# Kernel tuning notes

Measured on AMD Instinct MI355X. Metric: run time of the kernel, lower is better.

## Reference

```python
import jax, jax.numpy as jnp
import numpy as np

N, M, N0 = 100000, 12, 2500            # atoms, max neighbors, crystals
ORIG, C, NBR, H, NCONV = 92, 64, 41, 128, 3
EPS = 1e-5                              # torch BatchNorm1d default eps


def setup_inputs() -> dict:
    key = jax.random.key(0)
    ks = jax.random.split(key, 10)
    return {
        "atom_fea": jax.random.normal(ks[0], (N, ORIG), jnp.float32),
        "nbr_fea": jax.random.normal(ks[1], (N, M, NBR), jnp.float32),
        "nbr_fea_idx": jax.random.randint(ks[2], (N, M), 0, N),
        "crystal_atom_idx": jnp.sort(jax.random.randint(ks[3], (N,), 0, N0)),
        # learned parameters (Linear weights stored as (in, out))
        "emb_W": jax.random.normal(ks[4], (ORIG, C), jnp.float32) * 0.05,
        "emb_b": jnp.zeros((C,), jnp.float32),
        "fc_W": jax.random.normal(ks[5], (NCONV, 2 * C + NBR, 2 * C), jnp.float32) * 0.05,
        "fc_b": jnp.zeros((NCONV, 2 * C), jnp.float32),
        "bn1_g": jnp.ones((NCONV, 2 * C), jnp.float32),
        "bn1_b": jnp.zeros((NCONV, 2 * C), jnp.float32),
        "bn2_g": jnp.ones((NCONV, C), jnp.float32),
        "bn2_b": jnp.zeros((NCONV, C), jnp.float32),
        "head_W": jax.random.normal(ks[6], (C, H), jnp.float32) * 0.05,
        "head_b": jnp.zeros((H,), jnp.float32),
        "out_W": jax.random.normal(ks[7], (H, 1), jnp.float32) * 0.05,
        "out_b": jnp.zeros((1,), jnp.float32),
    }


def _bn(x, g, b):
    # training-mode BatchNorm1d: per-feature batch mean/var (biased)
    mu = jnp.mean(x, axis=0)
    var = jnp.var(x, axis=0)
    return (x - mu) * jax.lax.rsqrt(var + EPS) * g + b


def reference(atom_fea, nbr_fea, nbr_fea_idx, crystal_atom_idx,
              emb_W, emb_b, fc_W, fc_b, bn1_g, bn1_b, bn2_g, bn2_b,
              head_W, head_b, out_W, out_b):
    h = atom_fea @ emb_W + emb_b                       # (N, C)
    for l in range(NCONV):
        nbr_h = h[nbr_fea_idx]                         # gather (N, M, C)
        self_h = jnp.broadcast_to(h[:, None, :], (N, M, C))
        tot = jnp.concatenate([self_h, nbr_h, nbr_fea], axis=2)  # (N, M, 2C+NBR)
        g = tot @ fc_W[l] + fc_b[l]                    # (N, M, 2C)
        g = _bn(g.reshape(-1, 2 * C), bn1_g[l], bn1_b[l]).reshape(N, M, 2 * C)
        filt = jax.nn.sigmoid(g[..., :C])
        core = jax.nn.softplus(g[..., C:])
        summed = jnp.sum(filt * core, axis=1)          # (N, C)
        summed = _bn(summed, bn2_g[l], bn2_b[l])
        h = jax.nn.softplus(h + summed)                # residual
    # per-crystal mean pooling via segment sum
    counts = jax.ops.segment_sum(jnp.ones((N,), h.dtype), crystal_atom_idx, num_segments=N0)
    crys = jax.ops.segment_sum(h, crystal_atom_idx, num_segments=N0) / jnp.maximum(counts, 1.0)[:, None]
    z = jax.nn.softplus(jax.nn.softplus(crys) @ head_W + head_b)  # (N0, H)
    return z @ out_W + out_b                            # (N0, 1)
```

## Files before the change

### kernel.cpp

```cpp
#include <hip/hip_runtime.h>

#define NA 100000
#define MN 12
#define KE 41
#define N0C 2500
#define EPSBN 1e-5f
#define ROWDW 24
#define CONV_BLOCKS 1536
#define CONV_WAVES (CONV_BLOCKS * 4)

typedef _Float16 h2v __attribute__((ext_vector_type(2)));
typedef _Float16 h8v __attribute__((ext_vector_type(8)));
typedef float f4v __attribute__((ext_vector_type(4)));
typedef unsigned int uint;
union H2U { uint u; h2v h; };

__device__ __forceinline__ float softplusf(float x){
  float e = __expf(-fabsf(x));
  return fmaxf(x, 0.f) + __logf(1.f + e);
}
__device__ __forceinline__ float sigmoidf(float x){
  return __fdividef(1.f, 1.f + __expf(-x));
}
__device__ __forceinline__ int waveid(){
  return __builtin_amdgcn_readfirstlane((int)((blockIdx.x * blockDim.x + threadIdx.x) >> 6));
}

__global__ __launch_bounds__(256) void k_cast_e(const float* __restrict__ e,
                                                uint* __restrict__ EF)
{
  const int TOT = NA * MN * ROWDW;
  for (int i = blockIdx.x * 256 + threadIdx.x; i < TOT; i += gridDim.x * 256) {
    int r = i / ROWDW, k2 = i - r * ROWDW;
    const float* row = e + (size_t)r * KE;
    float a = 0.f, b = 0.f;
    if (k2 < 20) { a = row[2 * k2]; b = row[2 * k2 + 1]; }
    else if (k2 == 20) { a = row[40]; }
    H2U cv; cv.h = h2v{(_Float16)a, (_Float16)b};
    EF[i] = cv.u;
  }
}

__global__ __launch_bounds__(256) void k_embed(const float* __restrict__ af,
                                               const float* __restrict__ W,
                                               const float* __restrict__ b,
                                               float* __restrict__ h, int nw)
{
  int t = threadIdx.x & 63;
  int wid = waveid();
  float bias = b[t];
  for (int n0 = wid * 2; n0 < NA; n0 += nw * 2) {
    int n1 = n0 + 1;
    bool has1 = (n1 < NA);
    const float* a0 = af + (size_t)n0 * 92;
    const float* a1 = af + (size_t)(has1 ? n1 : n0) * 92;
    float acc0 = bias, acc1 = bias;
#pragma unroll 4
    for (int k = 0; k < 92; ++k) {
      float w = W[k * 64 + t];
      acc0 += a0[k] * w;
      acc1 += a1[k] * w;
    }
    h[(size_t)n0 * 64 + t] = acc0;
    if (has1) h[(size_t)n1 * 64 + t] = acc1;
  }
}

template<int FUSE>
__global__ __launch_bounds__(256) void k_hw(float* __restrict__ h,
                                            const float* __restrict__ summed,
                                            const float* __restrict__ scsh2,
                                            const float* __restrict__ fcW,
                                            uint* __restrict__ hWs,
                                            uint* __restrict__ hWn, int nw)
{
  __shared__ float Wl[64 * 256];
  for (int i = threadIdx.x; i < 64 * 256; i += 256) {
    int c = i >> 8, q = i & 255;
    int j = q & 63, part = q >> 6;
    Wl[(c * 64 + j) * 4 + part] = fcW[(c + ((part >> 1) << 6)) * 128 + ((part & 1) << 6) + j];
  }
  __syncthreads();
  int t = threadIdx.x & 63;
  int wid = waveid();
  float sc = 0.f, sh = 0.f;
  if (FUSE) { sc = scsh2[t]; sh = scsh2[64 + t]; }
  const float4* W4 = (const float4*)Wl;
  for (int n0 = wid * 2; n0 < NA; n0 += nw * 2) {
    int n1 = n0 + 1;
    bool has1 = (n1 < NA);
    float hf0 = h[(size_t)n0 * 64 + t];
    float hf1 = h[(size_t)(has1 ? n1 : n0) * 64 + t];
    if (FUSE) {
      hf0 = softplusf(hf0 + summed[(size_t)n0 * 64 + t] * sc + sh);
      hf1 = softplusf(hf1 + summed[(size_t)(has1 ? n1 : n0) * 64 + t] * sc + sh);
      h[(size_t)n0 * 64 + t] = hf0;
      if (has1) h[(size_t)n1 * 64 + t] = hf1;
    }
    float4 A = {0,0,0,0}, B = {0,0,0,0};
#pragma unroll 4
    for (int c = 0; c < 64; ++c) {
      float4 w = W4[c * 64 + t];
      float x0 = __shfl(hf0, c, 64);
      float x1 = __shfl(hf1, c, 64);
      A.x += x0 * w.x; A.y += x0 * w.y; A.z += x0 * w.z; A.w += x0 * w.w;
      B.x += x1 * w.x; B.y += x1 * w.y; B.z += x1 * w.z; B.w += x1 * w.w;
    }
    H2U p0, p1;
    p0.h = h2v{(_Float16)A.x, (_Float16)A.y};
    p1.h = h2v{(_Float16)A.z, (_Float16)A.w};
    hWs[(size_t)n0 * 64 + t] = p0.u;
    hWn[(size_t)n0 * 64 + t] = p1.u;
    if (has1) {
      p0.h = h2v{(_Float16)B.x, (_Float16)B.y};
      p1.h = h2v{(_Float16)B.z, (_Float16)B.w};
      hWs[(size_t)n1 * 64 + t] = p0.u;
      hWn[(size_t)n1 * 64 + t] = p1.u;
    }
  }
}

template<int APPLY>
__global__ __launch_bounds__(256) void k_conv(const uint* __restrict__ EF,
                                              const uint* __restrict__ hWs,
                                              const uint* __restrict__ hWn,
                                              const int*  __restrict__ idx,
                                              const float* __restrict__ We,
                                              const float* __restrict__ scsh,
                                              float* __restrict__ summed,
                                              float* __restrict__ stats)
{
  __shared__ float gt_all[4][12 * 132];
  int l = threadIdx.x & 63;
  int w = threadIdx.x >> 6;
  float* gt = gt_all[w];
  int wid = __builtin_amdgcn_readfirstlane(blockIdx.x * 4 + w);
  int c16 = l & 15, kg = l >> 4;

  h8v b1[8], b2[8];
#pragma unroll
  for (int T = 0; T < 8; ++T) {
    h8v v1 = {0,0,0,0,0,0,0,0}, v2 = {0,0,0,0,0,0,0,0};
#pragma unroll
    for (int j = 0; j < 8; ++j)
      v1[j] = (_Float16)We[(kg * 8 + j) * 128 + T * 16 + c16];
    if (kg < 2) {
#pragma unroll
      for (int j = 0; j < 8; ++j) {
        int k = 32 + kg * 8 + j;
        v2[j] = (k < KE) ? (_Float16)We[k * 128 + T * 16 + c16] : (_Float16)0.f;
      }
    }
    b1[T] = v1; b2[T] = v2;
  }

  float sc0 = 0, sh0 = 0, sc1 = 0, sh1 = 0;
  if (APPLY) { sc0 = scsh[l]; sc1 = scsh[l + 64]; sh0 = scsh[128 + l]; sh1 = scsh[192 + l]; }
  float s0 = 0, q0 = 0, s1 = 0, q1 = 0;

  for (int n = wid; n < NA; n += CONV_WAVES) {
    const uint* ep = EF + (size_t)n * (MN * ROWDW);
    h8v a1 = {0,0,0,0,0,0,0,0}, a2 = {0,0,0,0,0,0,0,0};
    if (c16 < MN) {
      a1 = *(const h8v*)(ep + c16 * ROWDW + kg * 4);
      if (kg < 2) a2 = *(const h8v*)(ep + c16 * ROWDW + 16 + kg * 4);
    }
    const int* ip = idx + n * MN;
    H2U sp; sp.u = hWs[(size_t)n * 64 + l];
    uint nbp[MN];
#pragma unroll
    for (int m = 0; m < MN; ++m) nbp[m] = hWn[(size_t)ip[m] * 64 + l];

    f4v acc[8];
#pragma unroll
    for (int T = 0; T < 8; ++T) acc[T] = f4v{0.f, 0.f, 0.f, 0.f};
#pragma unroll
    for (int T = 0; T < 8; ++T)
      acc[T] = __builtin_amdgcn_mfma_f32_16x16x32_f16(a1, b1[T], acc[T], 0, 0, 0);
#pragma unroll
    for (int T = 0; T < 8; ++T)
      acc[T] = __builtin_amdgcn_mfma_f32_16x16x32_f16(a2, b2[T], acc[T], 0, 0, 0);

    if (kg < 3) {
#pragma unroll
      for (int T = 0; T < 8; ++T)
#pragma unroll
        for (int r = 0; r < 4; ++r)
          gt[(kg * 4 + r) * 132 + T * 16 + c16] = acc[T][r];
    }

    float self0 = (float)sp.h[0], self1 = (float)sp.h[1];
    float accsum = 0.f;
#pragma unroll
    for (int m = 0; m < MN; ++m) {
      H2U nv; nv.u = nbp[m];
      float g0 = gt[m * 132 + l]      + self0 + (float)nv.h[0];
      float g1 = gt[m * 132 + 64 + l] + self1 + (float)nv.h[1];
      if (APPLY) {
        float f  = sigmoidf(g0 * sc0 + sh0);
        float cr = softplusf(g1 * sc1 + sh1);
        accsum += f * cr;
      } else {
        s0 += g0; q0 += g0 * g0;
        s1 += g1; q1 += g1 * g1;
      }
    }
    if (APPLY) {
      summed[(size_t)n * 64 + l] = accsum;
      s0 += accsum; q0 += accsum * accsum;
    }
  }
  if (APPLY) {
    atomicAdd(&stats[l], s0);
    atomicAdd(&stats[64 + l], q0);
  } else {
    atomicAdd(&stats[l], s0);
    atomicAdd(&stats[64 + l], s1);
    atomicAdd(&stats[128 + l], q0);
    atomicAdd(&stats[192 + l], q1);
  }
}

__global__ void k_fin1(const float* __restrict__ st, const float* __restrict__ g,
                       const float* __restrict__ b, float* __restrict__ scsh)
{
  int j = threadIdx.x;
  float inv = 1.f / (float)(NA * MN);
  float mean = st[j] * inv;
  float var  = st[128 + j] * inv - mean * mean;
  float rstd = rsqrtf(var + EPSBN);
  float sc = g[j] * rstd;
  scsh[j] = sc;
  scsh[128 + j] = b[j] - mean * sc;
}
__global__ void k_fin2(const float* __restrict__ st, const float* __restrict__ g,
                       const float* __restrict__ b, float* __restrict__ scsh)
{
  int j = threadIdx.x;
  float inv = 1.f / (float)NA;
  float mean = st[j] * inv;
  float var  = st[64 + j] * inv - mean * mean;
  float rstd = rsqrtf(var + EPSBN);
  float sc = g[j] * rstd;
  scsh[j] = sc;
  scsh[64 + j] = b[j] - mean * sc;
}

__global__ __launch_bounds__(256) void k_bn2res(float* __restrict__ h,
                                                const float* __restrict__ summed,
                                                const float* __restrict__ scsh)
{
  int tot = NA * 64 / 4;
  const float4* s4 = (const float4*)summed;
  float4* h4 = (float4*)h;
  for (int i = blockIdx.x * blockDim.x + threadIdx.x; i < tot; i += gridDim.x * blockDim.x) {
    int c4 = i & 15;
    float4 sc = ((const float4*)scsh)[c4];
    float4 sh = ((const float4*)(scsh + 64))[c4];
    float4 hv = h4[i], sv = s4[i];
    hv.x = softplusf(hv.x + sv.x * sc.x + sh.x);
    hv.y = softplusf(hv.y + sv.y * sc.y + sh.y);
    hv.z = softplusf(hv.z + sv.z * sc.z + sh.z);
    hv.w = softplusf(hv.w + sv.w * sc.w + sh.w);
    h4[i] = hv;
  }
}

__global__ __launch_bounds__(256) void k_pool(const float* __restrict__ h,
                                              const int* __restrict__ cidx,
                                              float* __restrict__ csum,
                                              float* __restrict__ ccnt, int nw)
{
  int t = threadIdx.x & 63;
  int wid = waveid();
  int chunk = (NA + nw - 1) / nw;
  int n0 = wid * chunk;
  int n1 = min(n0 + chunk, NA);
  if (n0 >= NA) return;
  float acc = 0.f, cacc = 0.f;
  int cur = -1;
  for (int n = n0; n < n1; ++n) {
    int ci = cidx[n];
    if (ci != cur) {
      if (cur >= 0) {
        atomicAdd(&csum[(size_t)cur * 64 + t], acc);
        if (t == 0) atomicAdd(&ccnt[cur], cacc);
      }
      cur = ci; acc = 0.f; cacc = 0.f;
    }
    acc += h[(size_t)n * 64 + t];
    cacc += 1.f;
  }
  if (cur >= 0) {
    atomicAdd(&csum[(size_t)cur * 64 + t], acc);
    if (t == 0) atomicAdd(&ccnt[cur], cacc);
  }
}

__global__ __launch_bounds__(256) void k_head(const float* __restrict__ csum,
                                              const float* __restrict__ ccnt,
                                              const float* __restrict__ Wh,
                                              const float* __restrict__ bh,
                                              const float* __restrict__ Wo,
                                              const float* __restrict__ bo,
                                              float* __restrict__ out)
{
  __shared__ float Wl[64 * 128];
  for (int i = threadIdx.x; i < 64 * 128; i += 256) Wl[i] = Wh[i];
  __syncthreads();
  int t = threadIdx.x & 63;
  int ci = blockIdx.x * 4 + (threadIdx.x >> 6);
  if (ci >= N0C) return;
  float cnt = fmaxf(ccnt[ci], 1.f);
  float x = softplusf(csum[(size_t)ci * 64 + t] / cnt);
  float acc0 = 0.f, acc1 = 0.f;
#pragma unroll 4
  for (int c = 0; c < 64; ++c) {
    float xc = __shfl(x, c, 64);
    acc0 += xc * Wl[c * 128 + t];
    acc1 += xc * Wl[c * 128 + 64 + t];
  }
  float z0 = softplusf(acc0 + bh[t]);
  float z1 = softplusf(acc1 + bh[64 + t]);
  float part = z0 * Wo[t] + z1 * Wo[64 + t];
#pragma unroll
  for (int s = 32; s >= 1; s >>= 1) part += __shfl_xor(part, s, 64);
  if (t == 0) out[ci] = part + bo[0];
}

extern "C" void kernel_launch(void* const* d_in, const int* in_sizes, int n_in,
                              void* d_out, int out_size, void* d_ws, size_t ws_size,
                              hipStream_t stream)
{
  const float* af    = (const float*)d_in[0];
  const float* nbr   = (const float*)d_in[1];
  const int*   nidx  = (const int*)d_in[2];
  const int*   cidx  = (const int*)d_in[3];
  const float* embW  = (const float*)d_in[4];
  const float* embB  = (const float*)d_in[5];
  const float* fcW   = (const float*)d_in[6];
  const float* bn1g  = (const float*)d_in[8];
  const float* bn1b  = (const float*)d_in[9];
  const float* bn2g  = (const float*)d_in[10];
  const float* bn2b  = (const float*)d_in[11];
  const float* headW = (const float*)d_in[12];
  const float* headB = (const float*)d_in[13];
  const float* outW  = (const float*)d_in[14];
  const float* outB  = (const float*)d_in[15];
  float* out = (float*)d_out;

  float* ws = (float*)d_ws;
  size_t off = 0;
  float* h      = ws + off; off += (size_t)NA * 64;
  uint*  hWs    = (uint*)(ws + off); off += (size_t)NA * 64;
  uint*  hWn    = (uint*)(ws + off); off += (size_t)NA * 64;
  uint*  EF     = (uint*)(ws + off); off += (size_t)NA * MN * ROWDW;
  float* summed = ws + off; off += (size_t)NA * 64;
  float* zr     = ws + off;
  float* stats1 = zr;
  float* stats2 = stats1 + 3 * 256;
  float* csum   = stats2 + 3 * 128;
  float* ccnt   = csum + (size_t)N0C * 64;
  size_t zcount = 3 * 256 + 3 * 128 + (size_t)N0C * 64 + N0C;
  float* scsh1  = ccnt + N0C;
  float* scsh2  = scsh1 + 3 * 256;

  hipMemsetAsync(zr, 0, zcount * sizeof(float), stream);

  k_cast_e<<<4096, 256, 0, stream>>>(nbr, EF);
  k_embed<<<512, 256, 0, stream>>>(af, embW, embB, h, 2048);

  for (int l = 0; l < 3; ++l) {
    const float* Wl = fcW + (size_t)l * 169 * 128;
    const float* We = Wl + 128 * 128;
    if (l == 0)
      k_hw<0><<<512, 256, 0, stream>>>(h, nullptr, nullptr, Wl, hWs, hWn, 2048);
    else
      k_hw<1><<<512, 256, 0, stream>>>(h, summed, scsh2 + (l - 1) * 128, Wl, hWs, hWn, 2048);
    k_conv<0><<<CONV_BLOCKS, 256, 0, stream>>>(EF, hWs, hWn, nidx, We, nullptr,
                                               nullptr, stats1 + l * 256);
    k_fin1<<<1, 128, 0, stream>>>(stats1 + l * 256, bn1g + l * 128, bn1b + l * 128,
                                  scsh1 + l * 256);
    k_conv<1><<<CONV_BLOCKS, 256, 0, stream>>>(EF, hWs, hWn, nidx, We, scsh1 + l * 256,
                                               summed, stats2 + l * 128);
    k_fin2<<<1, 64, 0, stream>>>(stats2 + l * 128, bn2g + l * 64, bn2b + l * 64,
                                 scsh2 + l * 128);
  }

  k_bn2res<<<2048, 256, 0, stream>>>(h, summed, scsh2 + 2 * 128);
  k_pool<<<512, 256, 0, stream>>>(h, cidx, csum, ccnt, 2048);
  k_head<<<625, 256, 0, stream>>>(csum, ccnt, headW, headB, outW, outB, out);
}
```

Before: 1.855 ms.

## Materialize pre-BN gate values in fp16 to skip recomputing conv pass

The first conv pass now stores the pre-BatchNorm gate values g0/g1 for every atom-neighbor pair as packed fp16 into a workspace buffer. A new k_gate kernel then streams that buffer to apply BN1, sigmoid, softplus and the neighbor sum, instead of rerunning the gather, MFMA and LDS stage a second time. The MFMA block is also moved ahead of the neighbor gather loads. This trades about 307 MB of extra write and read traffic per layer for removing the second random gather and matmul, and it rounds g to fp16 before the BN and activations. It falls back to the old path when the workspace is too small.

```diff
diff --git a/kernel.cpp b/kernel.cpp
--- a/kernel.cpp
+++ b/kernel.cpp
@@ -120,7 +120,7 @@
   }
 }
 
-template<int APPLY>
+template<int MODE>
 __global__ __launch_bounds__(256) void k_conv(const uint* __restrict__ EF,
                                               const uint* __restrict__ hWs,
                                               const uint* __restrict__ hWn,
@@ -128,7 +128,8 @@
                                               const float* __restrict__ We,
                                               const float* __restrict__ scsh,
                                               float* __restrict__ summed,
-                                              float* __restrict__ stats)
+                                              float* __restrict__ stats,
+                                              uint* __restrict__ g16)
 {
   __shared__ float gt_all[4][12 * 132];
   int l = threadIdx.x & 63;
@@ -155,7 +156,7 @@
   }
 
   float sc0 = 0, sh0 = 0, sc1 = 0, sh1 = 0;
-  if (APPLY) { sc0 = scsh[l]; sc1 = scsh[l + 64]; sh0 = scsh[128 + l]; sh1 = scsh[192 + l]; }
+  if (MODE == 1) { sc0 = scsh[l]; sc1 = scsh[l + 64]; sh0 = scsh[128 + l]; sh1 = scsh[192 + l]; }
   float s0 = 0, q0 = 0, s1 = 0, q1 = 0;
 
   for (int n = wid; n < NA; n += CONV_WAVES) {
@@ -165,52 +166,55 @@
       a1 = *(const h8v*)(ep + c16 * ROWDW + kg * 4);
       if (kg < 2) a2 = *(const h8v*)(ep + c16 * ROWDW + 16 + kg * 4);
     }
+    f4v acc[8];
+#pragma unroll
+    for (int T = 0; T < 8; ++T) acc[T] = f4v{0.f, 0.f, 0.f, 0.f};
+#pragma unroll
+    for (int T = 0; T < 8; ++T)
+      acc[T] = __builtin_amdgcn_mfma_f32_16x16x32_f16(a1, b1[T], acc[T], 0, 0, 0);
+#pragma unroll
+    for (int T = 0; T < 8; ++T)
+      acc[T] = __builtin_amdgcn_mfma_f32_16x16x32_f16(a2, b2[T], acc[T], 0, 0, 0);
+
+    if (kg < 3) {
+#pragma unroll
+      for (int T = 0; T < 8; ++T)
+#pragma unroll
+        for (int r = 0; r < 4; ++r)
+          gt[(kg * 4 + r) * 132 + T * 16 + c16] = acc[T][r];
+    }
+
     const int* ip = idx + n * MN;
     H2U sp; sp.u = hWs[(size_t)n * 64 + l];
+    float self0 = (float)sp.h[0], self1 = (float)sp.h[1];
     uint nbp[MN];
 #pragma unroll
     for (int m = 0; m < MN; ++m) nbp[m] = hWn[(size_t)ip[m] * 64 + l];
-
-    f4v acc[8];
-#pragma unroll
-    for (int T = 0; T < 8; ++T) acc[T] = f4v{0.f, 0.f, 0.f, 0.f};
-#pragma unroll
-    for (int T = 0; T < 8; ++T)
-      acc[T] = __builtin_amdgcn_mfma_f32_16x16x32_f16(a1, b1[T], acc[T], 0, 0, 0);
-#pragma unroll
-    for (int T = 0; T < 8; ++T)
-      acc[T] = __builtin_amdgcn_mfma_f32_16x16x32_f16(a2, b2[T], acc[T], 0, 0, 0);
-
-    if (kg < 3) {
-#pragma unroll
-      for (int T = 0; T < 8; ++T)
-#pragma unroll
-        for (int r = 0; r < 4; ++r)
-          gt[(kg * 4 + r) * 132 + T * 16 + c16] = acc[T][r];
-    }
-
-    float self0 = (float)sp.h[0], self1 = (float)sp.h[1];
     float accsum = 0.f;
 #pragma unroll
     for (int m = 0; m < MN; ++m) {
       H2U nv; nv.u = nbp[m];
       float g0 = gt[m * 132 + l]      + self0 + (float)nv.h[0];
       float g1 = gt[m * 132 + 64 + l] + self1 + (float)nv.h[1];
-      if (APPLY) {
+      if (MODE == 1) {
         float f  = sigmoidf(g0 * sc0 + sh0);
         float cr = softplusf(g1 * sc1 + sh1);
         accsum += f * cr;
       } else {
         s0 += g0; q0 += g0 * g0;
         s1 += g1; q1 += g1 * g1;
+        if (MODE == 2) {
+          H2U pk; pk.h = h2v{(_Float16)g0, (_Float16)g1};
+          g16[((size_t)n * MN + m) * 64 + l] = pk.u;
+        }
       }
     }
-    if (APPLY) {
+    if (MODE == 1) {
       summed[(size_t)n * 64 + l] = accsum;
       s0 += accsum; q0 += accsum * accsum;
     }
   }
-  if (APPLY) {
+  if (MODE == 1) {
     atomicAdd(&stats[l], s0);
     atomicAdd(&stats[64 + l], q0);
   } else {
@@ -219,6 +223,36 @@
     atomicAdd(&stats[128 + l], q0);
     atomicAdd(&stats[192 + l], q1);
   }
+}
+
+__global__ __launch_bounds__(256) void k_gate(const uint* __restrict__ g16,
+                                              const float* __restrict__ scsh,
+                                              float* __restrict__ summed,
+                                              float* __restrict__ stats, int nw)
+{
+  int l = threadIdx.x & 63;
+  int wid = waveid();
+  float sc0 = scsh[l], sc1 = scsh[l + 64];
+  float sh0 = scsh[128 + l], sh1 = scsh[192 + l];
+  float bs = 0.f, bq = 0.f;
+  for (int n = wid; n < NA; n += nw) {
+    const uint* gp = g16 + (size_t)n * MN * 64 + l;
+    uint u[MN];
+#pragma unroll
+    for (int m = 0; m < MN; ++m) u[m] = gp[m * 64];
+    float accsum = 0.f;
+#pragma unroll
+    for (int m = 0; m < MN; ++m) {
+      H2U gv; gv.u = u[m];
+      float f  = sigmoidf((float)gv.h[0] * sc0 + sh0);
+      float cr = softplusf((float)gv.h[1] * sc1 + sh1);
+      accsum += f * cr;
+    }
+    summed[(size_t)n * 64 + l] = accsum;
+    bs += accsum; bq += accsum * accsum;
+  }
+  atomicAdd(&stats[l], bs);
+  atomicAdd(&stats[64 + l], bq);
 }
 
 __global__ void k_fin1(const float* __restrict__ st, const float* __restrict__ g,
@@ -364,6 +398,10 @@
   size_t zcount = 3 * 256 + 3 * 128 + (size_t)N0C * 64 + N0C;
   float* scsh1  = ccnt + N0C;
   float* scsh2  = scsh1 + 3 * 256;
+  off += zcount + 3 * 256 + 3 * 128;
+  uint* g16 = (uint*)(ws + off);
+  size_t need_g = (off + (size_t)NA * MN * 64) * sizeof(float);
+  bool use_g = (ws_size >= need_g);
 
   hipMemsetAsync(zr, 0, zcount * sizeof(float), stream);
 
@@ -377,12 +415,21 @@
       k_hw<0><<<512, 256, 0, stream>>>(h, nullptr, nullptr, Wl, hWs, hWn, 2048);
     else
       k_hw<1><<<512, 256, 0, stream>>>(h, summed, scsh2 + (l - 1) * 128, Wl, hWs, hWn, 2048);
-    k_conv<0><<<CONV_BLOCKS, 256, 0, stream>>>(EF, hWs, hWn, nidx, We, nullptr,
-                                               nullptr, stats1 + l * 256);
-    k_fin1<<<1, 128, 0, stream>>>(stats1 + l * 256, bn1g + l * 128, bn1b + l * 128,
-                                  scsh1 + l * 256);
-    k_conv<1><<<CONV_BLOCKS, 256, 0, stream>>>(EF, hWs, hWn, nidx, We, scsh1 + l * 256,
-                                               summed, stats2 + l * 128);
+    if (use_g) {
+      k_conv<2><<<CONV_BLOCKS, 256, 0, stream>>>(EF, hWs, hWn, nidx, We, nullptr,
+                                                 nullptr, stats1 + l * 256, g16);
+      k_fin1<<<1, 128, 0, stream>>>(stats1 + l * 256, bn1g + l * 128, bn1b + l * 128,
+                                    scsh1 + l * 256);
+      k_gate<<<2048, 256, 0, stream>>>(g16, scsh1 + l * 256, summed,
+                                       stats2 + l * 128, 8192);
+    } else {
+      k_conv<0><<<CONV_BLOCKS, 256, 0, stream>>>(EF, hWs, hWn, nidx, We, nullptr,
+                                                 nullptr, stats1 + l * 256, nullptr);
+      k_fin1<<<1, 128, 0, stream>>>(stats1 + l * 256, bn1g + l * 128, bn1b + l * 128,
+                                    scsh1 + l * 256);
+      k_conv<1><<<CONV_BLOCKS, 256, 0, stream>>>(EF, hWs, hWn, nidx, We, scsh1 + l * 256,
+                                                 summed, stats2 + l * 128, nullptr);
+    }
     k_fin2<<<1, 64, 0, stream>>>(stats2 + l * 128, bn2g + l * 64, bn2b + l * 64,
                                  scsh2 + l * 128);
   }
```

After: 2.008 ms. 1.08x slower.

## Stage edge-weight B operands in LDS and pack gate tile as fp16 pairs

Applied to the files above, without the earlier changes.

Moves the transposed edge-feature weight matrix from 16 per-lane h8v register fragments into a padded LDS array. Each MFMA step now reads its B operand from LDS, cutting VGPR pressure so more waves can be resident. The per-wave gate scratch is converted to packed fp16 pairs (cvt_pkrtz), which halves LDS footprint and the number of reads in the gating loop. The gather loads are moved after the MFMA block, and the grid is reduced to 1280 blocks. The trade-offs are extra LDS traffic per atom, an fp16 rounding of the edge partial sums before the BN statistics, and an in-kernel weight staging prologue with a barrier.

```diff
diff --git a/kernel.cpp b/kernel.cpp
--- a/kernel.cpp
+++ b/kernel.cpp
@@ -6,14 +6,17 @@
 #define N0C 2500
 #define EPSBN 1e-5f
 #define ROWDW 24
-#define CONV_BLOCKS 1536
+#define CONV_BLOCKS 1280
 #define CONV_WAVES (CONV_BLOCKS * 4)
+#define WEP 72
+#define GTP 66
 
 typedef _Float16 h2v __attribute__((ext_vector_type(2)));
 typedef _Float16 h8v __attribute__((ext_vector_type(8)));
+typedef __fp16 fp16x2 __attribute__((ext_vector_type(2)));
 typedef float f4v __attribute__((ext_vector_type(4)));
 typedef unsigned int uint;
-union H2U { uint u; h2v h; };
+union H2U { uint u; h2v h; fp16x2 p; };
 
 __device__ __forceinline__ float softplusf(float x){
   float e = __expf(-fabsf(x));
@@ -120,7 +123,7 @@
   }
 }
 
-template<int APPLY>
+template<int MODE>
 __global__ __launch_bounds__(256) void k_conv(const uint* __restrict__ EF,
                                               const uint* __restrict__ hWs,
                                               const uint* __restrict__ hWn,
@@ -130,32 +133,27 @@
                                               float* __restrict__ summed,
                                               float* __restrict__ stats)
 {
-  __shared__ float gt_all[4][12 * 132];
-  int l = threadIdx.x & 63;
-  int w = threadIdx.x >> 6;
-  float* gt = gt_all[w];
+  __shared__ _Float16 WeT[128 * WEP];
+  __shared__ uint gt_all[4][12 * GTP];
+  int tid = threadIdx.x;
+  for (int i = tid; i < 128 * (WEP / 2); i += 256) {
+    int col = i / (WEP / 2), k2 = i - col * (WEP / 2);
+    int k0 = 2 * k2, k1 = 2 * k2 + 1;
+    float a = (k0 < KE) ? We[k0 * 128 + col] : 0.f;
+    float b = (k1 < KE) ? We[k1 * 128 + col] : 0.f;
+    H2U pk; pk.h = h2v{(_Float16)a, (_Float16)b};
+    *(uint*)&WeT[col * WEP + 2 * k2] = pk.u;
+  }
+  __syncthreads();
+
+  int l = tid & 63;
+  int w = tid >> 6;
+  uint* gt = gt_all[w];
   int wid = __builtin_amdgcn_readfirstlane(blockIdx.x * 4 + w);
   int c16 = l & 15, kg = l >> 4;
 
-  h8v b1[8], b2[8];
-#pragma unroll
-  for (int T = 0; T < 8; ++T) {
-    h8v v1 = {0,0,0,0,0,0,0,0}, v2 = {0,0,0,0,0,0,0,0};
-#pragma unroll
-    for (int j = 0; j < 8; ++j)
-      v1[j] = (_Float16)We[(kg * 8 + j) * 128 + T * 16 + c16];
-    if (kg < 2) {
-#pragma unroll
-      for (int j = 0; j < 8; ++j) {
-        int k = 32 + kg * 8 + j;
-        v2[j] = (k < KE) ? (_Float16)We[k * 128 + T * 16 + c16] : (_Float16)0.f;
-      }
-    }
-    b1[T] = v1; b2[T] = v2;
-  }
-
   float sc0 = 0, sh0 = 0, sc1 = 0, sh1 = 0;
-  if (APPLY) { sc0 = scsh[l]; sc1 = scsh[l + 64]; sh0 = scsh[128 + l]; sh1 = scsh[192 + l]; }
+  if (MODE == 1) { sc0 = scsh[l]; sc1 = scsh[l + 64]; sh0 = scsh[128 + l]; sh1 = scsh[192 + l]; }
   float s0 = 0, q0 = 0, s1 = 0, q1 = 0;
 
   for (int n = wid; n < NA; n += CONV_WAVES) {
@@ -165,38 +163,44 @@
       a1 = *(const h8v*)(ep + c16 * ROWDW + kg * 4);
       if (kg < 2) a2 = *(const h8v*)(ep + c16 * ROWDW + 16 + kg * 4);
     }
+    f4v acc[8];
+#pragma unroll
+    for (int T = 0; T < 8; ++T) acc[T] = f4v{0.f, 0.f, 0.f, 0.f};
+#pragma unroll
+    for (int T = 0; T < 8; ++T) {
+      h8v b = *(const h8v*)&WeT[(T * 16 + c16) * WEP + kg * 8];
+      acc[T] = __builtin_amdgcn_mfma_f32_16x16x32_f16(a1, b, acc[T], 0, 0, 0);
+    }
+#pragma unroll
+    for (int T = 0; T < 8; ++T) {
+      h8v b = *(const h8v*)&WeT[(T * 16 + c16) * WEP + 32 + kg * 8];
+      acc[T] = __builtin_amdgcn_mfma_f32_16x16x32_f16(a2, b, acc[T], 0, 0, 0);
+    }
+
+    if (kg < 3) {
+#pragma unroll
+      for (int T = 0; T < 4; ++T)
+#pragma unroll
+        for (int r = 0; r < 4; ++r) {
+          H2U u; u.p = __builtin_amdgcn_cvt_pkrtz(acc[T][r], acc[T + 4][r]);
+          gt[(kg * 4 + r) * GTP + T * 16 + c16] = u.u;
+        }
+    }
+
     const int* ip = idx + n * MN;
     H2U sp; sp.u = hWs[(size_t)n * 64 + l];
+    float self0 = (float)sp.h[0], self1 = (float)sp.h[1];
     uint nbp[MN];
 #pragma unroll
     for (int m = 0; m < MN; ++m) nbp[m] = hWn[(size_t)ip[m] * 64 + l];
-
-    f4v acc[8];
-#pragma unroll
-    for (int T = 0; T < 8; ++T) acc[T] = f4v{0.f, 0.f, 0.f, 0.f};
-#pragma unroll
-    for (int T = 0; T < 8; ++T)
-      acc[T] = __builtin_amdgcn_mfma_f32_16x16x32_f16(a1, b1[T], acc[T], 0, 0, 0);
-#pragma unroll
-    for (int T = 0; T < 8; ++T)
-      acc[T] = __builtin_amdgcn_mfma_f32_16x16x32_f16(a2, b2[T], acc[T], 0, 0, 0);
-
-    if (kg < 3) {
-#pragma unroll
-      for (int T = 0; T < 8; ++T)
-#pragma unroll
-        for (int r = 0; r < 4; ++r)
-          gt[(kg * 4 + r) * 132 + T * 16 + c16] = acc[T][r];
-    }
-
-    float self0 = (float)sp.h[0], self1 = (float)sp.h[1];
     float accsum = 0.f;
 #pragma unroll
     for (int m = 0; m < MN; ++m) {
       H2U nv; nv.u = nbp[m];
-      float g0 = gt[m * 132 + l]      + self0 + (float)nv.h[0];
-      float g1 = gt[m * 132 + 64 + l] + self1 + (float)nv.h[1];
-      if (APPLY) {
+      H2U gv; gv.u = gt[m * GTP + l];
+      float g0 = (float)gv.h[0] + self0 + (float)nv.h[0];
+      float g1 = (float)gv.h[1] + self1 + (float)nv.h[1];
+      if (MODE == 1) {
         float f  = sigmoidf(g0 * sc0 + sh0);
         float cr = softplusf(g1 * sc1 + sh1);
         accsum += f * cr;
@@ -205,12 +209,12 @@
         s1 += g1; q1 += g1 * g1;
       }
     }
-    if (APPLY) {
+    if (MODE == 1) {
       summed[(size_t)n * 64 + l] = accsum;
       s0 += accsum; q0 += accsum * accsum;
     }
   }
-  if (APPLY) {
+  if (MODE == 1) {
     atomicAdd(&stats[l], s0);
     atomicAdd(&stats[64 + l], q0);
   } else {
```

After: 1.726 ms. -7.0%, faster.
